# Performance work log

Measured on AMD Instinct MI355X. Metric: run time of the kernel, lower is better.

The kernel has to match this reference:

```python
import jax, jax.numpy as jnp
import numpy as np

N, IN_F, OUT_F = 8192, 256, 256
ALPHA = 0.2  # LeakyReLU negative slope


def setup_inputs() -> dict:
    key = jax.random.key(0)
    k1, k2, k3, k4 = jax.random.split(key, 4)
    x = jax.random.normal(k1, (N, IN_F), dtype=jnp.float32)
    adj = jax.random.randint(k2, (N, N), 0, 2, dtype=jnp.int32)
    # xavier-uniform-ish params
    lim_w = np.sqrt(6.0 / (OUT_F + IN_F)) * np.sqrt(2.0)
    w = jax.random.uniform(k3, (OUT_F, IN_F), jnp.float32, -lim_w, lim_w)
    lim_a = np.sqrt(6.0 / (2 * OUT_F + 1)) * np.sqrt(2.0)
    a = jax.random.uniform(k4, (2 * OUT_F, 1), jnp.float32, -lim_a, lim_a)
    return {"adj": adj, "x": x, "w": w, "a": a}


def reference(adj, x, w, a):
    h = x @ w.T                                   # [N, F]
    a1 = a[:OUT_F, 0]                             # [F]
    a2 = a[OUT_F:, 0]                             # [F]
    # score[i,j] = h_i . a1 + h_j . a2  (equivalent to concat([h_i,h_j]) @ a,
    # without materializing the O(N^2 * 2F) concat tensor)
    scores = (h @ a1)[:, None] + (h @ a2)[None, :]  # [N, N]
    key_ = jax.nn.leaky_relu(scores, negative_slope=ALPHA)
    masked = jnp.where(adj > 0, key_, jnp.zeros((), key_.dtype))
    attn = jax.nn.softmax(masked, axis=1)         # [N, N]
    h_prime = attn @ h                            # [N, F]
    return jax.nn.elu(h_prime)
```

## Files before the change

### kernel.cpp

```cpp
#include <hip/hip_runtime.h>

typedef short  short8  __attribute__((ext_vector_type(8)));
typedef short  short4v __attribute__((ext_vector_type(4)));
typedef float  float4v __attribute__((ext_vector_type(4)));
typedef int    int4v   __attribute__((ext_vector_type(4)));
typedef int    int2v   __attribute__((ext_vector_type(2)));

#define LOG2E 1.4426950408889634f

static __device__ __forceinline__ short f2bf(float f) {
  unsigned u = __builtin_bit_cast(unsigned, f);
  u = (u + 0x7fffu + ((u >> 16) & 1u)) >> 16;
  return (short)u;
}
static __device__ __forceinline__ float bf2f(short s) {
  return __builtin_bit_cast(float, ((unsigned)(unsigned short)s) << 16);
}

typedef __attribute__((address_space(3))) char  as3c;
typedef __attribute__((address_space(1))) char  as1c;
static __device__ __forceinline__ void dma16(const void* g, void* l) {
  __builtin_amdgcn_global_load_lds((const as1c*)g, (as3c*)l, 16, 0, 0);
}

__global__ __launch_bounds__(256) void k_hgemm(
    const float* __restrict__ x, const float* __restrict__ w,
    short* __restrict__ hT, float* __restrict__ hTf) {
  const int I0   = blockIdx.x * 64;
  const int lane = threadIdx.x & 63;
  const int wn   = threadIdx.x >> 6;
  const int lrow = lane & 15;
  const int lk8  = (lane >> 4) << 3;

  float4v zero4 = {0.f, 0.f, 0.f, 0.f};
  float4v acc[4][4];
  #pragma unroll
  for (int mi = 0; mi < 4; ++mi)
    #pragma unroll
    for (int ni = 0; ni < 4; ++ni) acc[mi][ni] = zero4;

  for (int k0 = 0; k0 < 256; k0 += 32) {
    short8 ah[4], al[4], bh[4], bl[4];
    #pragma unroll
    for (int mi = 0; mi < 4; ++mi) {
      const float* xp = x + (size_t)(I0 + mi * 16 + lrow) * 256 + k0 + lk8;
      float4v va = *(const float4v*)xp;
      float4v vb = *(const float4v*)(xp + 4);
      #pragma unroll
      for (int e = 0; e < 4; ++e) {
        short h = f2bf(va[e]); ah[mi][e] = h;     al[mi][e]     = f2bf(va[e] - bf2f(h));
        h = f2bf(vb[e]);       ah[mi][4 + e] = h; al[mi][4 + e] = f2bf(vb[e] - bf2f(h));
      }
    }
    #pragma unroll
    for (int ni = 0; ni < 4; ++ni) {
      const float* wp = w + (size_t)(wn * 64 + ni * 16 + lrow) * 256 + k0 + lk8;
      float4v va = *(const float4v*)wp;
      float4v vb = *(const float4v*)(wp + 4);
      #pragma unroll
      for (int e = 0; e < 4; ++e) {
        short h = f2bf(va[e]); bh[ni][e] = h;     bl[ni][e]     = f2bf(va[e] - bf2f(h));
        h = f2bf(vb[e]);       bh[ni][4 + e] = h; bl[ni][4 + e] = f2bf(vb[e] - bf2f(h));
      }
    }
    #pragma unroll
    for (int mi = 0; mi < 4; ++mi)
      #pragma unroll
      for (int ni = 0; ni < 4; ++ni) {
        acc[mi][ni] = __builtin_amdgcn_mfma_f32_16x16x32_bf16(al[mi], bh[ni], acc[mi][ni], 0, 0, 0);
        acc[mi][ni] = __builtin_amdgcn_mfma_f32_16x16x32_bf16(ah[mi], bl[ni], acc[mi][ni], 0, 0, 0);
        acc[mi][ni] = __builtin_amdgcn_mfma_f32_16x16x32_bf16(ah[mi], bh[ni], acc[mi][ni], 0, 0, 0);
      }
  }
  const int r0 = (lane >> 4) << 2;
  #pragma unroll
  for (int mi = 0; mi < 4; ++mi)
    #pragma unroll
    for (int ni = 0; ni < 4; ++ni) {
      const int c   = wn * 64 + ni * 16 + lrow;
      const int row = I0 + mi * 16 + r0;
      float4v v = acc[mi][ni];
      short4v sv;
      #pragma unroll
      for (int r = 0; r < 4; ++r) sv[r] = f2bf(v[r]);
      *(short4v*)(hT + (size_t)c * 8192 + row) = sv;
      *(float4v*)(hTf + (size_t)c * 8192 + row) = v;
    }
}

__global__ __launch_bounds__(256) void k_scores1(
    const float* __restrict__ hTf, const float* __restrict__ a,
    float* __restrict__ t1p, float* __restrict__ t2p) {
  const int i = blockIdx.x * 256 + threadIdx.x;
  const int q = blockIdx.y;
  float s1 = 0.f, s2 = 0.f;
  #pragma unroll 8
  for (int kf = q * 128; kf < q * 128 + 128; ++kf) {
    float hv = hTf[(size_t)kf * 8192 + i];
    s1 = fmaf(hv, a[kf], s1);
    s2 = fmaf(hv, a[256 + kf], s2);
  }
  t1p[q * 8192 + i] = s1;
  t2p[q * 8192 + i] = s2;
}

__global__ __launch_bounds__(256) void k_scores2(
    const float* __restrict__ t1p, const float* __restrict__ t2p,
    float2* __restrict__ e1f1, float2* __restrict__ ef2) {
  const int i = blockIdx.x * 256 + threadIdx.x;
  const float t1 = LOG2E * (t1p[i] + t1p[8192 + i]);
  const float t2 = LOG2E * (t2p[i] + t2p[8192 + i]);
  e1f1[i] = make_float2(exp2f(t1), exp2f(0.2f * t1));
  ef2[i]  = make_float2(exp2f(t2), exp2f(0.2f * t2));
}

__global__ __launch_bounds__(512) void k_gat(
    const int* __restrict__ adj, const short* __restrict__ hT,
    const float2* __restrict__ e1f1, const float2* __restrict__ ef2,
    float* __restrict__ Np, float* __restrict__ Zp) {
  __shared__ __align__(16) char Wt[2][17408];
  __shared__ __align__(16) char Hb[2][32768];
  __shared__ __align__(16) char Elds[16384];

  const int tid = threadIdx.x, lane = tid & 63, wave = tid >> 6;
  const int wm = wave >> 2, wn = wave & 3;
  const int lrow = lane & 15, lk16 = (lane >> 4) << 4;
  const int I0 = blockIdx.x * 128;
  const int j0 = blockIdx.y * 2048;

  const int ar = tid >> 4, aj = tid & 15;
  const int* agp = adj + (size_t)(I0 + ar) * 8192 + j0 + aj * 4;
  float e1p[4], f1p[4];
  #pragma unroll
  for (int p = 0; p < 4; ++p) {
    float2 v = e1f1[I0 + p * 32 + ar];
    e1p[p] = v.x; f1p[p] = v.y;
  }
  const int wwo = ar * 136 + aj * 8;

  const int l8 = lane >> 3, l7 = lane & 7;
  const short* hdma = hT + (size_t)(wave * 32 + l8) * 8192 + j0 + (l7 ^ l8) * 8;
  const int hlo = wave * 4096;

  const int ardo = (wm * 64 + lrow) * 136 + lk16;
  const int brdo = (wn * 64 + lrow) * 128;
  const int c0   = ((lane >> 4) ^ (lrow & 7)) << 4;

  float4v zero4 = {0.f, 0.f, 0.f, 0.f};
  float4v acc[4][4];
  #pragma unroll
  for (int mi = 0; mi < 4; ++mi)
    #pragma unroll
    for (int ni = 0; ni < 4; ++ni) acc[mi][ni] = zero4;
  float zacc[4] = {0.f, 0.f, 0.f, 0.f};
  int4v ga[4];

#define WCOMP(T, DST)                                                         \
  { const float4v ge0 = *(const float4v*)(Elds + (T) * 512 + aj * 32);        \
    const float4v ge1 = *(const float4v*)(Elds + (T) * 512 + aj * 32 + 16);   \
    _Pragma("unroll")                                                         \
    for (int p = 0; p < 4; ++p) {                                             \
      float w0 = ga[p][0] ? fmaxf(e1p[p] * ge0[0], f1p[p] * ge0[1]) : 1.0f;   \
      float w1 = ga[p][1] ? fmaxf(e1p[p] * ge0[2], f1p[p] * ge0[3]) : 1.0f;   \
      float w2 = ga[p][2] ? fmaxf(e1p[p] * ge1[0], f1p[p] * ge1[1]) : 1.0f;   \
      float w3 = ga[p][3] ? fmaxf(e1p[p] * ge1[2], f1p[p] * ge1[3]) : 1.0f;   \
      zacc[p] += (w0 + w1) + (w2 + w3);                                       \
      int2v pw;                                                               \
      asm("v_cvt_pk_bf16_f32 %0, %1, %2" : "=v"(pw[0]) : "v"(w0), "v"(w1));   \
      asm("v_cvt_pk_bf16_f32 %0, %1, %2" : "=v"(pw[1]) : "v"(w2), "v"(w3));   \
      *(int2v*)((DST) + wwo + p * 4352) = pw;                                 \
    } }

  {
    const char* esrc = (const char*)(ef2 + j0);
    *(float4v*)(Elds + tid * 32)      = *(const float4v*)(esrc + tid * 32);
    *(float4v*)(Elds + tid * 32 + 16) = *(const float4v*)(esrc + tid * 32 + 16);
  }
  __syncthreads();
  #pragma unroll
  for (int p = 0; p < 4; ++p)
    ga[p] = __builtin_nontemporal_load((const int4v*)(agp + (size_t)p * 262144));
  __builtin_amdgcn_sched_barrier(0);
  #pragma unroll
  for (int q = 0; q < 4; ++q)
    dma16(hdma + q * 65536, Hb[0] + hlo + q * 1024);
  __builtin_amdgcn_sched_barrier(0);
  WCOMP(0, Wt[0]);
  #pragma unroll
  for (int p = 0; p < 4; ++p)
    ga[p] = __builtin_nontemporal_load((const int4v*)(agp + (size_t)p * 262144 + 64));
  __builtin_amdgcn_sched_barrier(0);
  asm volatile("s_waitcnt vmcnt(4) lgkmcnt(0)" ::: "memory");
  __builtin_amdgcn_s_barrier();
  __builtin_amdgcn_sched_barrier(0);

  #pragma unroll 2
  for (int s = 0; s < 32; ++s) {
    const int cur = s & 1, nx = cur ^ 1;
    if (s < 31) {
      const int so = (s + 1) * 64;
      #pragma unroll
      for (int q = 0; q < 4; ++q)
        dma16(hdma + so + q * 65536, Hb[nx] + hlo + q * 1024);
    }
    __builtin_amdgcn_sched_barrier(0);
    short8 af[4], bf[4];
    #pragma unroll
    for (int mi = 0; mi < 4; ++mi) af[mi] = *(const short8*)(Wt[cur] + ardo + mi * 2176);
    #pragma unroll
    for (int ni = 0; ni < 4; ++ni) bf[ni] = *(const short8*)(Hb[cur] + brdo + ni * 2048 + c0);
    #pragma unroll
    for (int mi = 0; mi < 4; ++mi)
      #pragma unroll
      for (int ni = 0; ni < 4; ++ni)
        acc[mi][ni] = __builtin_amdgcn_mfma_f32_16x16x32_bf16(af[mi], bf[ni], acc[mi][ni], 0, 0, 0);
    if (s < 31) WCOMP(s + 1, Wt[nx]);
    if (s < 31) {
      const int sp = (s + 2 < 32) ? s + 2 : 31;
      const int so = sp * 64;
      #pragma unroll
      for (int p = 0; p < 4; ++p)
        ga[p] = __builtin_nontemporal_load((const int4v*)(agp + (size_t)p * 262144 + so));
    }
    __builtin_amdgcn_sched_barrier(0);
    #pragma unroll
    for (int mi = 0; mi < 4; ++mi) af[mi] = *(const short8*)(Wt[cur] + ardo + mi * 2176 + 64);
    #pragma unroll
    for (int ni = 0; ni < 4; ++ni) bf[ni] = *(const short8*)(Hb[cur] + brdo + ni * 2048 + (c0 ^ 64));
    #pragma unroll
    for (int mi = 0; mi < 4; ++mi)
      #pragma unroll
      for (int ni = 0; ni < 4; ++ni)
        acc[mi][ni] = __builtin_amdgcn_mfma_f32_16x16x32_bf16(af[mi], bf[ni], acc[mi][ni], 0, 0, 0);
    if (s < 31) {
      asm volatile("s_waitcnt vmcnt(4) lgkmcnt(0)" ::: "memory");
      __builtin_amdgcn_s_barrier();
      __builtin_amdgcn_sched_barrier(0);
    }
  }
#undef WCOMP

  __syncthreads();
  float* zl = (float*)Elds;
  #pragma unroll
  for (int p = 0; p < 4; ++p) zl[(ar + p * 32) * 16 + aj] = zacc[p];
  __syncthreads();
  if (tid < 128) {
    float z = 0.f;
    #pragma unroll
    for (int g = 0; g < 16; ++g) z += zl[tid * 16 + g];
    Zp[(size_t)blockIdx.y * 8192 + I0 + tid] = z;
  }

  float* Npb = Np + (size_t)blockIdx.y * 2097152;
  const int r0 = (lane >> 4) << 2;
  #pragma unroll
  for (int mi = 0; mi < 4; ++mi) {
    const int rowb = I0 + wm * 64 + mi * 16 + r0;
    #pragma unroll
    for (int ni = 0; ni < 4; ++ni) {
      const int col = wn * 64 + ni * 16 + lrow;
      #pragma unroll
      for (int r = 0; r < 4; ++r)
        Npb[(size_t)(rowb + r) * 256 + col] = acc[mi][ni][r];
    }
  }
}

__global__ __launch_bounds__(256) void k_out(
    const float* __restrict__ Np, const float* __restrict__ Zp,
    float* __restrict__ out) {
  const int idx = blockIdx.x * 256 + threadIdx.x;
  const int i = idx >> 6;
  float z = 0.f;
  #pragma unroll
  for (int y = 0; y < 4; ++y) z += Zp[y * 8192 + i];
  float4v n = {0.f, 0.f, 0.f, 0.f};
  #pragma unroll
  for (int y = 0; y < 4; ++y) {
    float4v v = ((const float4v*)Np)[(size_t)y * 524288 + idx];
    #pragma unroll
    for (int e = 0; e < 4; ++e) n[e] += v[e];
  }
  const float rz = 1.0f / z;
  float4v o;
  #pragma unroll
  for (int e = 0; e < 4; ++e) {
    float v = n[e] * rz;
    o[e] = (v > 0.f) ? v : expm1f(v);
  }
  ((float4v*)out)[idx] = o;
}

extern "C" void kernel_launch(void* const* d_in, const int* in_sizes, int n_in,
                              void* d_out, int out_size, void* d_ws, size_t ws_size,
                              hipStream_t stream) {
  const int*   adj = (const int*)d_in[0];
  const float* x   = (const float*)d_in[1];
  const float* w   = (const float*)d_in[2];
  const float* a   = (const float*)d_in[3];
  float* out = (float*)d_out;

  char* ws = (char*)d_ws;
  short*  hT   = (short*)(ws + 0);
  float*  t1p  = (float*)(ws + 4194304);
  float*  t2p  = (float*)(ws + 4259840);
  float2* e1f1 = (float2*)(ws + 4325376);
  float2* ef2  = (float2*)(ws + 4390912);
  float*  Zp   = (float*)(ws + 4456448);
  float*  Np   = (float*)(ws + 16777216);
  float*  hTf  = (float*)d_out;

  k_hgemm  <<<128, 256, 0, stream>>>(x, w, hT, hTf);
  k_scores1<<<dim3(32, 2), 256, 0, stream>>>(hTf, a, t1p, t2p);
  k_scores2<<<32, 256, 0, stream>>>(t1p, t2p, e1f1, ef2);
  k_gat    <<<dim3(64, 4), 512, 0, stream>>>(adj, hT, e1f1, ef2, Np, Zp);
  k_out    <<<2048, 256, 0, stream>>>(Np, Zp, out);
}
```

Before: 126.0 us.

## Split GAT j-range eight ways with halved K-step and smaller LDS tiles

Doubles the j-split of the attention kernel from 4 to 8 blocks per row tile (512 blocks instead of 256) and halves the per-step K chunk to 32 columns, shrinking LDS buffers and re-deriving the swizzled layouts, the adjacency-load mapping and the weight computation per thread. It adds launch_bounds occupancy hints and s_setprio around the MFMA block. The aim is more blocks per device and higher occupancy to better hide adjacency and hT load latency. The cost is twice the partial-sum traffic for Np/Zp and more reduction work in k_out.

```diff
diff --git a/kernel.cpp b/kernel.cpp
--- a/kernel.cpp
+++ b/kernel.cpp
@@ -114,37 +114,34 @@
   ef2[i]  = make_float2(exp2f(t2), exp2f(0.2f * t2));
 }
 
-__global__ __launch_bounds__(512) void k_gat(
+__global__ __launch_bounds__(512, 4) void k_gat(
     const int* __restrict__ adj, const short* __restrict__ hT,
     const float2* __restrict__ e1f1, const float2* __restrict__ ef2,
     float* __restrict__ Np, float* __restrict__ Zp) {
-  __shared__ __align__(16) char Wt[2][17408];
-  __shared__ __align__(16) char Hb[2][32768];
-  __shared__ __align__(16) char Elds[16384];
+  __shared__ __align__(16) char Wt[2][11264];
+  __shared__ __align__(16) char Hb[2][16384];
+  __shared__ __align__(16) char Elds[9216];
 
   const int tid = threadIdx.x, lane = tid & 63, wave = tid >> 6;
   const int wm = wave >> 2, wn = wave & 3;
-  const int lrow = lane & 15, lk16 = (lane >> 4) << 4;
+  const int lrow = lane & 15;
   const int I0 = blockIdx.x * 128;
-  const int j0 = blockIdx.y * 2048;
-
-  const int ar = tid >> 4, aj = tid & 15;
-  const int* agp = adj + (size_t)(I0 + ar) * 8192 + j0 + aj * 4;
-  float e1p[4], f1p[4];
-  #pragma unroll
-  for (int p = 0; p < 4; ++p) {
-    float2 v = e1f1[I0 + p * 32 + ar];
-    e1p[p] = v.x; f1p[p] = v.y;
-  }
-  const int wwo = ar * 136 + aj * 8;
-
-  const int l8 = lane >> 3, l7 = lane & 7;
-  const short* hdma = hT + (size_t)(wave * 32 + l8) * 8192 + j0 + (l7 ^ l8) * 8;
-  const int hlo = wave * 4096;
-
-  const int ardo = (wm * 64 + lrow) * 136 + lk16;
-  const int brdo = (wn * 64 + lrow) * 128;
-  const int c0   = ((lane >> 4) ^ (lrow & 7)) << 4;
+  const int j0 = blockIdx.y * 1024;
+
+  const int ar = tid >> 2, ac = tid & 3;
+  const int* agp = adj + (size_t)(I0 + ar) * 8192 + j0 + ac * 8;
+  float e1v, f1v;
+  { float2 v = e1f1[I0 + ar]; e1v = v.x; f1v = v.y; }
+  const int wwo = ar * 88 + ac * 16;
+  const int ec72 = ac * 72;
+
+  const short* hdma = hT + (size_t)(wave * 32 + (lane >> 2)) * 8192 + j0
+                    + (((lane & 3) ^ ((lane >> 3) & 3)) << 3);
+  const int hlo = wave * 2048;
+
+  const int ardo = (wm * 64 + lrow) * 88 + ((lane >> 4) << 4);
+  const int brdo = (wn * 64 + lrow) * 64
+                 + (((lane >> 4) ^ ((lrow >> 1) & 3)) << 4);
 
   float4v zero4 = {0.f, 0.f, 0.f, 0.f};
   float4v acc[4][4];
@@ -152,45 +149,48 @@
   for (int mi = 0; mi < 4; ++mi)
     #pragma unroll
     for (int ni = 0; ni < 4; ++ni) acc[mi][ni] = zero4;
-  float zacc[4] = {0.f, 0.f, 0.f, 0.f};
-  int4v ga[4];
+  float zacc = 0.f;
+  int4v ga0, ga1;
 
 #define WCOMP(T, DST)                                                         \
-  { const float4v ge0 = *(const float4v*)(Elds + (T) * 512 + aj * 32);        \
-    const float4v ge1 = *(const float4v*)(Elds + (T) * 512 + aj * 32 + 16);   \
-    _Pragma("unroll")                                                         \
-    for (int p = 0; p < 4; ++p) {                                             \
-      float w0 = ga[p][0] ? fmaxf(e1p[p] * ge0[0], f1p[p] * ge0[1]) : 1.0f;   \
-      float w1 = ga[p][1] ? fmaxf(e1p[p] * ge0[2], f1p[p] * ge0[3]) : 1.0f;   \
-      float w2 = ga[p][2] ? fmaxf(e1p[p] * ge1[0], f1p[p] * ge1[1]) : 1.0f;   \
-      float w3 = ga[p][3] ? fmaxf(e1p[p] * ge1[2], f1p[p] * ge1[3]) : 1.0f;   \
-      zacc[p] += (w0 + w1) + (w2 + w3);                                       \
-      int2v pw;                                                               \
-      asm("v_cvt_pk_bf16_f32 %0, %1, %2" : "=v"(pw[0]) : "v"(w0), "v"(w1));   \
-      asm("v_cvt_pk_bf16_f32 %0, %1, %2" : "=v"(pw[1]) : "v"(w2), "v"(w3));   \
-      *(int2v*)((DST) + wwo + p * 4352) = pw;                                 \
-    } }
+  { const char* eb = Elds + (T) * 288 + ec72;                                 \
+    const float4v E0 = *(const float4v*)(eb);                                 \
+    const float4v E1 = *(const float4v*)(eb + 16);                            \
+    const float4v E2 = *(const float4v*)(eb + 32);                            \
+    const float4v E3 = *(const float4v*)(eb + 48);                            \
+    float w0 = ga0[0] ? fmaxf(e1v * E0[0], f1v * E0[1]) : 1.0f;               \
+    float w1 = ga0[1] ? fmaxf(e1v * E0[2], f1v * E0[3]) : 1.0f;               \
+    float w2 = ga0[2] ? fmaxf(e1v * E1[0], f1v * E1[1]) : 1.0f;               \
+    float w3 = ga0[3] ? fmaxf(e1v * E1[2], f1v * E1[3]) : 1.0f;               \
+    float w4 = ga1[0] ? fmaxf(e1v * E2[0], f1v * E2[1]) : 1.0f;               \
+    float w5 = ga1[1] ? fmaxf(e1v * E2[2], f1v * E2[3]) : 1.0f;               \
+    float w6 = ga1[2] ? fmaxf(e1v * E3[0], f1v * E3[1]) : 1.0f;               \
+    float w7 = ga1[3] ? fmaxf(e1v * E3[2], f1v * E3[3]) : 1.0f;               \
+    zacc += ((w0 + w1) + (w2 + w3)) + ((w4 + w5) + (w6 + w7));                \
+    int4v pw;                                                                 \
+    asm("v_cvt_pk_bf16_f32 %0, %1, %2" : "=v"(pw[0]) : "v"(w0), "v"(w1));     \
+    asm("v_cvt_pk_bf16_f32 %0, %1, %2" : "=v"(pw[1]) : "v"(w2), "v"(w3));     \
+    asm("v_cvt_pk_bf16_f32 %0, %1, %2" : "=v"(pw[2]) : "v"(w4), "v"(w5));     \
+    asm("v_cvt_pk_bf16_f32 %0, %1, %2" : "=v"(pw[3]) : "v"(w6), "v"(w7));     \
+    *(int4v*)((DST) + wwo) = pw; }
 
   {
-    const char* esrc = (const char*)(ef2 + j0);
-    *(float4v*)(Elds + tid * 32)      = *(const float4v*)(esrc + tid * 32);
-    *(float4v*)(Elds + tid * 32 + 16) = *(const float4v*)(esrc + tid * 32 + 16);
+    const int b = tid >> 2;
+    *(float4v*)(Elds + (b >> 2) * 288 + (b & 3) * 72 + (tid & 3) * 16) =
+        *(const float4v*)((const char*)(ef2 + j0) + tid * 16);
   }
   __syncthreads();
-  #pragma unroll
-  for (int p = 0; p < 4; ++p)
-    ga[p] = __builtin_nontemporal_load((const int4v*)(agp + (size_t)p * 262144));
+  ga0 = __builtin_nontemporal_load((const int4v*)(agp));
+  ga1 = __builtin_nontemporal_load((const int4v*)(agp + 4));
   __builtin_amdgcn_sched_barrier(0);
-  #pragma unroll
-  for (int q = 0; q < 4; ++q)
-    dma16(hdma + q * 65536, Hb[0] + hlo + q * 1024);
+  dma16(hdma, Hb[0] + hlo);
+  dma16(hdma + 131072, Hb[0] + hlo + 1024);
   __builtin_amdgcn_sched_barrier(0);
   WCOMP(0, Wt[0]);
-  #pragma unroll
-  for (int p = 0; p < 4; ++p)
-    ga[p] = __builtin_nontemporal_load((const int4v*)(agp + (size_t)p * 262144 + 64));
+  ga0 = __builtin_nontemporal_load((const int4v*)(agp + 32));
+  ga1 = __builtin_nontemporal_load((const int4v*)(agp + 36));
   __builtin_amdgcn_sched_barrier(0);
-  asm volatile("s_waitcnt vmcnt(4) lgkmcnt(0)" ::: "memory");
+  asm volatile("s_waitcnt vmcnt(2) lgkmcnt(0)" ::: "memory");
   __builtin_amdgcn_s_barrier();
   __builtin_amdgcn_sched_barrier(0);
 
@@ -198,42 +198,32 @@
   for (int s = 0; s < 32; ++s) {
     const int cur = s & 1, nx = cur ^ 1;
     if (s < 31) {
-      const int so = (s + 1) * 64;
-      #pragma unroll
-      for (int q = 0; q < 4; ++q)
-        dma16(hdma + so + q * 65536, Hb[nx] + hlo + q * 1024);
+      const int so = (s + 1) * 32;
+      dma16(hdma + so, Hb[nx] + hlo);
+      dma16(hdma + so + 131072, Hb[nx] + hlo + 1024);
     }
     __builtin_amdgcn_sched_barrier(0);
     short8 af[4], bf[4];
     #pragma unroll
-    for (int mi = 0; mi < 4; ++mi) af[mi] = *(const short8*)(Wt[cur] + ardo + mi * 2176);
-    #pragma unroll
-    for (int ni = 0; ni < 4; ++ni) bf[ni] = *(const short8*)(Hb[cur] + brdo + ni * 2048 + c0);
+    for (int mi = 0; mi < 4; ++mi) af[mi] = *(const short8*)(Wt[cur] + ardo + mi * 1408);
+    #pragma unroll
+    for (int ni = 0; ni < 4; ++ni) bf[ni] = *(const short8*)(Hb[cur] + brdo + ni * 1024);
+    __builtin_amdgcn_s_setprio(1);
     #pragma unroll
     for (int mi = 0; mi < 4; ++mi)
       #pragma unroll
       for (int ni = 0; ni < 4; ++ni)
         acc[mi][ni] = __builtin_amdgcn_mfma_f32_16x16x32_bf16(af[mi], bf[ni], acc[mi][ni], 0, 0, 0);
+    __builtin_amdgcn_s_setprio(0);
     if (s < 31) WCOMP(s + 1, Wt[nx]);
     if (s < 31) {
       const int sp = (s + 2 < 32) ? s + 2 : 31;
-      const int so = sp * 64;
-      #pragma unroll
-      for (int p = 0; p < 4; ++p)
-        ga[p] = __builtin_nontemporal_load((const int4v*)(agp + (size_t)p * 262144 + so));
+      ga0 = __builtin_nontemporal_load((const int4v*)(agp + sp * 32));
+      ga1 = __builtin_nontemporal_load((const int4v*)(agp + sp * 32 + 4));
     }
     __builtin_amdgcn_sched_barrier(0);
-    #pragma unroll
-    for (int mi = 0; mi < 4; ++mi) af[mi] = *(const short8*)(Wt[cur] + ardo + mi * 2176 + 64);
-    #pragma unroll
-    for (int ni = 0; ni < 4; ++ni) bf[ni] = *(const short8*)(Hb[cur] + brdo + ni * 2048 + (c0 ^ 64));
-    #pragma unroll
-    for (int mi = 0; mi < 4; ++mi)
-      #pragma unroll
-      for (int ni = 0; ni < 4; ++ni)
-        acc[mi][ni] = __builtin_amdgcn_mfma_f32_16x16x32_bf16(af[mi], bf[ni], acc[mi][ni], 0, 0, 0);
     if (s < 31) {
-      asm volatile("s_waitcnt vmcnt(4) lgkmcnt(0)" ::: "memory");
+      asm volatile("s_waitcnt vmcnt(2) lgkmcnt(0)" ::: "memory");
       __builtin_amdgcn_s_barrier();
       __builtin_amdgcn_sched_barrier(0);
     }
@@ -242,13 +232,10 @@
 
   __syncthreads();
   float* zl = (float*)Elds;
-  #pragma unroll
-  for (int p = 0; p < 4; ++p) zl[(ar + p * 32) * 16 + aj] = zacc[p];
+  zl[ar * 4 + ac] = zacc;
   __syncthreads();
   if (tid < 128) {
-    float z = 0.f;
-    #pragma unroll
-    for (int g = 0; g < 16; ++g) z += zl[tid * 16 + g];
+    float z = zl[tid * 4] + zl[tid * 4 + 1] + zl[tid * 4 + 2] + zl[tid * 4 + 3];
     Zp[(size_t)blockIdx.y * 8192 + I0 + tid] = z;
   }
 
@@ -274,10 +261,10 @@
   const int i = idx >> 6;
   float z = 0.f;
   #pragma unroll
-  for (int y = 0; y < 4; ++y) z += Zp[y * 8192 + i];
+  for (int y = 0; y < 8; ++y) z += Zp[y * 8192 + i];
   float4v n = {0.f, 0.f, 0.f, 0.f};
   #pragma unroll
-  for (int y = 0; y < 4; ++y) {
+  for (int y = 0; y < 8; ++y) {
     float4v v = ((const float4v*)Np)[(size_t)y * 524288 + idx];
     #pragma unroll
     for (int e = 0; e < 4; ++e) n[e] += v[e];
@@ -314,6 +301,6 @@
   k_hgemm  <<<128, 256, 0, stream>>>(x, w, hT, hTf);
   k_scores1<<<dim3(32, 2), 256, 0, stream>>>(hTf, a, t1p, t2p);
   k_scores2<<<32, 256, 0, stream>>>(t1p, t2p, e1f1, ef2);
-  k_gat    <<<dim3(64, 4), 512, 0, stream>>>(adj, hT, e1f1, ef2, Np, Zp);
+  k_gat    <<<dim3(64, 8), 512, 0, stream>>>(adj, hT, e1f1, ef2, Np, Zp);
   k_out    <<<2048, 256, 0, stream>>>(Np, Zp, out);
 }
```

Result: slower. 178.3 us (+41.6%).

## Fuse score projections into h GEMM epilogue and remap GAT block order

Applied to the files above, without the earlier changes.

Computes the h·a1 and h·a2 projections inside the h GEMM epilogue from the fp32 accumulators, reducing through shared memory. This removes the fp32 hT buffer write and the separate k_scores1 launch that re-read it. The GEMM tile shrinks to 32 rows so twice as many blocks fill the GPU. The GAT kernel also remaps block ids so the four j-slices of one row block run adjacently, which may improve cache reuse of adj and e1f1.

```diff
diff --git a/kernel.cpp b/kernel.cpp
--- a/kernel.cpp
+++ b/kernel.cpp
@@ -25,24 +25,35 @@
 
 __global__ __launch_bounds__(256) void k_hgemm(
     const float* __restrict__ x, const float* __restrict__ w,
-    short* __restrict__ hT, float* __restrict__ hTf) {
-  const int I0   = blockIdx.x * 64;
-  const int lane = threadIdx.x & 63;
-  const int wn   = threadIdx.x >> 6;
+    const float* __restrict__ a, short* __restrict__ hT,
+    float* __restrict__ s1, float* __restrict__ s2) {
+  __shared__ float zl1[2048], zl2[2048];
+  const int I0   = blockIdx.x * 32;
+  const int tid  = threadIdx.x;
+  const int lane = tid & 63;
+  const int wn   = tid >> 6;
   const int lrow = lane & 15;
   const int lk8  = (lane >> 4) << 3;
 
+  float a1c[4], a2c[4];
+  #pragma unroll
+  for (int ni = 0; ni < 4; ++ni) {
+    const int col = wn * 64 + ni * 16 + lrow;
+    a1c[ni] = a[col];
+    a2c[ni] = a[256 + col];
+  }
+
   float4v zero4 = {0.f, 0.f, 0.f, 0.f};
-  float4v acc[4][4];
-  #pragma unroll
-  for (int mi = 0; mi < 4; ++mi)
+  float4v acc[2][4];
+  #pragma unroll
+  for (int mi = 0; mi < 2; ++mi)
     #pragma unroll
     for (int ni = 0; ni < 4; ++ni) acc[mi][ni] = zero4;
 
   for (int k0 = 0; k0 < 256; k0 += 32) {
-    short8 ah[4], al[4], bh[4], bl[4];
-    #pragma unroll
-    for (int mi = 0; mi < 4; ++mi) {
+    short8 ah[2], al[2], bh[4], bl[4];
+    #pragma unroll
+    for (int mi = 0; mi < 2; ++mi) {
       const float* xp = x + (size_t)(I0 + mi * 16 + lrow) * 256 + k0 + lk8;
       float4v va = *(const float4v*)xp;
       float4v vb = *(const float4v*)(xp + 4);
@@ -64,7 +75,7 @@
       }
     }
     #pragma unroll
-    for (int mi = 0; mi < 4; ++mi)
+    for (int mi = 0; mi < 2; ++mi)
       #pragma unroll
       for (int ni = 0; ni < 4; ++ni) {
         acc[mi][ni] = __builtin_amdgcn_mfma_f32_16x16x32_bf16(al[mi], bh[ni], acc[mi][ni], 0, 0, 0);
@@ -72,9 +83,10 @@
         acc[mi][ni] = __builtin_amdgcn_mfma_f32_16x16x32_bf16(ah[mi], bh[ni], acc[mi][ni], 0, 0, 0);
       }
   }
+
   const int r0 = (lane >> 4) << 2;
   #pragma unroll
-  for (int mi = 0; mi < 4; ++mi)
+  for (int mi = 0; mi < 2; ++mi) {
     #pragma unroll
     for (int ni = 0; ni < 4; ++ni) {
       const int c   = wn * 64 + ni * 16 + lrow;
@@ -84,32 +96,41 @@
       #pragma unroll
       for (int r = 0; r < 4; ++r) sv[r] = f2bf(v[r]);
       *(short4v*)(hT + (size_t)c * 8192 + row) = sv;
-      *(float4v*)(hTf + (size_t)c * 8192 + row) = v;
-    }
-}
-
-__global__ __launch_bounds__(256) void k_scores1(
-    const float* __restrict__ hTf, const float* __restrict__ a,
-    float* __restrict__ t1p, float* __restrict__ t2p) {
-  const int i = blockIdx.x * 256 + threadIdx.x;
-  const int q = blockIdx.y;
-  float s1 = 0.f, s2 = 0.f;
-  #pragma unroll 8
-  for (int kf = q * 128; kf < q * 128 + 128; ++kf) {
-    float hv = hTf[(size_t)kf * 8192 + i];
-    s1 = fmaf(hv, a[kf], s1);
-    s2 = fmaf(hv, a[256 + kf], s2);
-  }
-  t1p[q * 8192 + i] = s1;
-  t2p[q * 8192 + i] = s2;
+    }
+    #pragma unroll
+    for (int r = 0; r < 4; ++r) {
+      const int srow = mi * 16 + r0 + r;
+      float p1 = 0.f, p2 = 0.f;
+      #pragma unroll
+      for (int ni = 0; ni < 4; ++ni) {
+        p1 = fmaf(acc[mi][ni][r], a1c[ni], p1);
+        p2 = fmaf(acc[mi][ni][r], a2c[ni], p2);
+      }
+      const int gcol = wn * 16 + lrow;
+      zl1[srow * 64 + gcol] = p1;
+      zl2[srow * 64 + gcol] = p2;
+    }
+  }
+  __syncthreads();
+  if (tid < 32) {
+    float v1 = 0.f, v2 = 0.f;
+    #pragma unroll
+    for (int g = 0; g < 64; ++g) {
+      const int gg = (g + tid) & 63;
+      v1 += zl1[tid * 64 + gg];
+      v2 += zl2[tid * 64 + gg];
+    }
+    s1[I0 + tid] = v1;
+    s2[I0 + tid] = v2;
+  }
 }
 
 __global__ __launch_bounds__(256) void k_scores2(
-    const float* __restrict__ t1p, const float* __restrict__ t2p,
+    const float* __restrict__ s1, const float* __restrict__ s2,
     float2* __restrict__ e1f1, float2* __restrict__ ef2) {
   const int i = blockIdx.x * 256 + threadIdx.x;
-  const float t1 = LOG2E * (t1p[i] + t1p[8192 + i]);
-  const float t2 = LOG2E * (t2p[i] + t2p[8192 + i]);
+  const float t1 = LOG2E * s1[i];
+  const float t2 = LOG2E * s2[i];
   e1f1[i] = make_float2(exp2f(t1), exp2f(0.2f * t1));
   ef2[i]  = make_float2(exp2f(t2), exp2f(0.2f * t2));
 }
@@ -125,8 +146,10 @@
   const int tid = threadIdx.x, lane = tid & 63, wave = tid >> 6;
   const int wm = wave >> 2, wn = wave & 3;
   const int lrow = lane & 15, lk16 = (lane >> 4) << 4;
-  const int I0 = blockIdx.x * 128;
-  const int j0 = blockIdx.y * 2048;
+  const int bid = blockIdx.y * 64 + blockIdx.x;
+  const int bx = bid >> 2, by = bid & 3;
+  const int I0 = bx * 128;
+  const int j0 = by * 2048;
 
   const int ar = tid >> 4, aj = tid & 15;
   const int* agp = adj + (size_t)(I0 + ar) * 8192 + j0 + aj * 4;
@@ -249,10 +272,10 @@
     float z = 0.f;
     #pragma unroll
     for (int g = 0; g < 16; ++g) z += zl[tid * 16 + g];
-    Zp[(size_t)blockIdx.y * 8192 + I0 + tid] = z;
-  }
-
-  float* Npb = Np + (size_t)blockIdx.y * 2097152;
+    Zp[(size_t)by * 8192 + I0 + tid] = z;
+  }
+
+  float* Npb = Np + (size_t)by * 2097152;
   const int r0 = (lane >> 4) << 2;
   #pragma unroll
   for (int mi = 0; mi < 4; ++mi) {
@@ -303,17 +326,15 @@
 
   char* ws = (char*)d_ws;
   short*  hT   = (short*)(ws + 0);
-  float*  t1p  = (float*)(ws + 4194304);
-  float*  t2p  = (float*)(ws + 4259840);
+  float*  s1   = (float*)(ws + 4194304);
+  float*  s2   = (float*)(ws + 4259840);
   float2* e1f1 = (float2*)(ws + 4325376);
   float2* ef2  = (float2*)(ws + 4390912);
   float*  Zp   = (float*)(ws + 4456448);
   float*  Np   = (float*)(ws + 16777216);
-  float*  hTf  = (float*)d_out;
-
-  k_hgemm  <<<128, 256, 0, stream>>>(x, w, hT, hTf);
-  k_scores1<<<dim3(32, 2), 256, 0, stream>>>(hTf, a, t1p, t2p);
-  k_scores2<<<32, 256, 0, stream>>>(t1p, t2p, e1f1, ef2);
+
+  k_hgemm  <<<256, 256, 0, stream>>>(x, w, a, hT, s1, s2);
+  k_scores2<<<32, 256, 0, stream>>>(s1, s2, e1f1, ef2);
   k_gat    <<<dim3(64, 4), 512, 0, stream>>>(adj, hT, e1f1, ef2, Np, Zp);
   k_out    <<<2048, 256, 0, stream>>>(Np, Zp, out);
 }
```

Result: faster. 103.7 us, median of 3 (-17.7%).
